# Kernel optimization log

Hardware: AMD Instinct MI355X
Metric: run time of the kernel (lower is better)

Reference implementation:

```python
import jax, jax.numpy as jnp
import numpy as np

D = 64          # dim1 = dim2 = dim3
B = 512         # batch
MMHID = 256
F = (D + 1) ** 3  # 274625, encoder1 input size
SKIP = 3 * (D + 1)  # 195


def _lin(x, w, b):
    # torch nn.Linear: y = x @ W^T + b, W: [out, in]
    return x @ w.T + b


def _bilinear(x1, x2, w, b):
    # torch nn.Bilinear: y_o = x1_i W_{oij} x2_j + b_o
    return jnp.einsum('bi,oij,bj->bo', x1, w, x2) + b


def setup_inputs() -> dict:
    key = jax.random.key(0)
    ks = jax.random.split(key, 16)

    def n(k, shape, scale):
        return (jax.random.normal(k, shape, dtype=jnp.float32) * scale)

    inp = {
        'vec1': n(ks[0], (B, D), 1.0),
        'vec2': n(ks[1], (B, D), 1.0),
        'vec3': n(ks[2], (B, D), 1.0),
        # gated branch 1
        'h1_w': n(ks[3], (D, D), 1.0 / np.sqrt(D)), 'h1_b': jnp.zeros((D,), jnp.float32),
        'z1_w': n(ks[4], (D, D, D), 1.0 / D), 'z1_b': jnp.zeros((D,), jnp.float32),
        'o1_w': n(ks[5], (D, D), 1.0 / np.sqrt(D)), 'o1_b': jnp.zeros((D,), jnp.float32),
        # gated branch 2
        'h2_w': n(ks[6], (D, D), 1.0 / np.sqrt(D)), 'h2_b': jnp.zeros((D,), jnp.float32),
        'z2_w': n(ks[7], (D, D, D), 1.0 / D), 'z2_b': jnp.zeros((D,), jnp.float32),
        'o2_w': n(ks[8], (D, D), 1.0 / np.sqrt(D)), 'o2_b': jnp.zeros((D,), jnp.float32),
        # gated branch 3
        'h3_w': n(ks[9], (D, D), 1.0 / np.sqrt(D)), 'h3_b': jnp.zeros((D,), jnp.float32),
        'z3_w': n(ks[10], (D, D, D), 1.0 / D), 'z3_b': jnp.zeros((D,), jnp.float32),
        'o3_w': n(ks[11], (D, D), 1.0 / np.sqrt(D)), 'o3_b': jnp.zeros((D,), jnp.float32),
        # encoders
        'enc1_w': n(ks[12], (MMHID, F), 1.0 / np.sqrt(F)), 'enc1_b': jnp.zeros((MMHID,), jnp.float32),
        'enc2_w': n(ks[13], (MMHID, MMHID + SKIP), 1.0 / np.sqrt(MMHID + SKIP)), 'enc2_b': jnp.zeros((MMHID,), jnp.float32),
    }
    return inp


def reference(vec1, vec2, vec3,
              h1_w, h1_b, z1_w, z1_b, o1_w, o1_b,
              h2_w, h2_b, z2_w, z2_b, o2_w, o2_b,
              h3_w, h3_b, z3_w, z3_b, o3_w, o3_b,
              enc1_w, enc1_b, enc2_w, enc2_b):
    # dropout layers are identity in eval mode
    h1 = jax.nn.relu(_lin(vec1, h1_w, h1_b))
    z1 = _bilinear(vec1, vec3, z1_w, z1_b)
    o1 = jax.nn.relu(_lin(jax.nn.sigmoid(z1) * h1, o1_w, o1_b))

    h2 = jax.nn.relu(_lin(vec2, h2_w, h2_b))
    z2 = _bilinear(vec2, vec3, z2_w, z2_b)
    o2 = jax.nn.relu(_lin(jax.nn.sigmoid(z2) * h2, o2_w, o2_b))

    h3 = jax.nn.relu(_lin(vec3, h3_w, h3_b))
    z3 = _bilinear(vec1, vec3, z3_w, z3_b)  # note: z3 uses (vec1, vec3) per source
    o3 = jax.nn.relu(_lin(jax.nn.sigmoid(z3) * h3, o3_w, o3_b))

    ones = jnp.ones((o1.shape[0], 1), o1.dtype)
    o1 = jnp.concatenate([o1, ones], axis=1)  # [B, D+1]
    o2 = jnp.concatenate([o2, ones], axis=1)
    o3 = jnp.concatenate([o3, ones], axis=1)

    # trilinear outer product, flattened in (i, j, k) order matching
    # bmm(o1, o2).flatten then bmm(., o3).flatten in torch
    o123 = jnp.einsum('bi,bj,bk->bijk', o1, o2, o3).reshape(o1.shape[0], -1)  # [B, F]

    out = jax.nn.relu(_lin(o123, enc1_w, enc1_b))
    out = jnp.concatenate([out, o1, o2, o3], axis=1)  # skip connection
    out = jax.nn.relu(_lin(out, enc2_w, enc2_b))
    return out
```

## Files before the change

### kernel.cpp

```cpp
#include <hip/hip_runtime.h>
#include <hip/hip_bf16.h>
#include <stdint.h>

typedef unsigned short u16;
typedef unsigned int u32;

#define F1 274625
#define IJ1 4225

typedef float v4f __attribute__((ext_vector_type(4)));
typedef __bf16 v8bf __attribute__((ext_vector_type(8)));

__device__ __forceinline__ float lof(u32 u) { union { u32 u; float f; } c; c.u = u << 16; return c.f; }
__device__ __forceinline__ u16 f2bf(float f) {
  union { float f; u32 u; } c; c.f = f;
  u32 r = (c.u >> 16) & 1u;
  return (u16)((c.u + 0x7fffu + r) >> 16);
}
__device__ __forceinline__ u32 pkbf(u32 a, u32 b) {
  union { float f; u32 u; } ca, cb; ca.u = a; cb.u = b;
  __hip_bfloat162 h = __float22bfloat162_rn(make_float2(ca.f, cb.f));
  union { __hip_bfloat162 h; u32 u; } c; c.h = h; return c.u;
}

__global__ void __launch_bounds__(256) k0_transpose(const float* __restrict__ v1,
    const float* __restrict__ v2, const float* __restrict__ v3, float* __restrict__ xT) {
  int g = blockIdx.x * 256 + threadIdx.x;
  if (g >= 3 * 64 * 512) return;
  int t = g >> 15, r = g & 32767;
  int d = r >> 9, b = r & 511;
  const float* v = (t == 0) ? v1 : ((t == 1) ? v2 : v3);
  xT[g] = v[b * 64 + d];
}

__global__ void __launch_bounds__(256) k1_bilinear(
    const float* __restrict__ zw1, const float* __restrict__ zw2, const float* __restrict__ zw3,
    const float* __restrict__ xT, float* __restrict__ zsum) {
  int bid = blockIdx.x;
  int bh = bid & 1, o = (bid >> 1) & 63, t = bid >> 7;
  int b = bh * 256 + threadIdx.x;
  const float* zw = (t == 0) ? zw1 : ((t == 1) ? zw2 : zw3);
  const float* xiT = xT + ((t == 1) ? 32768 : 0);
  const float* x3T = xT + 65536;
  float x3r[64];
#pragma unroll
  for (int j = 0; j < 64; ++j) x3r[j] = x3T[j * 512 + b];
  const float4* w4 = (const float4*)(zw + o * 4096);
  float acc = 0.f;
#pragma unroll 4
  for (int i = 0; i < 64; ++i) {
    float xi = xiT[i * 512 + b];
    float s = 0.f;
#pragma unroll
    for (int q = 0; q < 16; ++q) {
      float4 w = w4[i * 16 + q];
      s += w.x * x3r[q*4+0] + w.y * x3r[q*4+1] + w.z * x3r[q*4+2] + w.w * x3r[q*4+3];
    }
    acc += xi * s;
  }
  zsum[t * 32768 + o * 512 + b] = acc;
}

__global__ void __launch_bounds__(256) k2_branch(
    const float* __restrict__ hw1, const float* __restrict__ hb1,
    const float* __restrict__ ow1, const float* __restrict__ ob1,
    const float* __restrict__ hw2, const float* __restrict__ hb2,
    const float* __restrict__ ow2, const float* __restrict__ ob2,
    const float* __restrict__ hw3, const float* __restrict__ hb3,
    const float* __restrict__ ow3, const float* __restrict__ ob3,
    const float* __restrict__ zb1, const float* __restrict__ zb2, const float* __restrict__ zb3,
    const float* __restrict__ xT, const float* __restrict__ zsum,
    float* __restrict__ oT, u16* __restrict__ o3row) {
  int t = blockIdx.x >> 3, bc = blockIdx.x & 7;
  int lane = threadIdx.x & 63;
  int w = __builtin_amdgcn_readfirstlane((int)(threadIdx.x >> 6));
  int b = bc * 64 + lane;
  const float* hw = (t==0)?hw1:((t==1)?hw2:hw3);
  const float* hb = (t==0)?hb1:((t==1)?hb2:hb3);
  const float* ow = (t==0)?ow1:((t==1)?ow2:ow3);
  const float* ob = (t==0)?ob1:((t==1)?ob2:ob3);
  const float* zb = (t==0)?zb1:((t==1)?zb2:zb3);
  const float* xtT = xT + t * 32768;
  const float4* hw4 = (const float4*)hw;
  const float4* ow4 = (const float4*)ow;
  __shared__ float gT[64][68];
  float xr[64];
#pragma unroll
  for (int k = 0; k < 64; ++k) xr[k] = xtT[k * 512 + b];
#pragma unroll
  for (int ii = 0; ii < 16; ii += 4) {
    float gv[4];
#pragma unroll
    for (int q = 0; q < 4; ++q) {
      int i = w * 16 + ii + q;
      float a = hb[i];
#pragma unroll
      for (int kq = 0; kq < 16; ++kq) {
        float4 h4 = hw4[i * 16 + kq];
        a += h4.x * xr[kq*4+0] + h4.y * xr[kq*4+1] + h4.z * xr[kq*4+2] + h4.w * xr[kq*4+3];
      }
      float hv = fmaxf(a, 0.f);
      float z = zsum[t * 32768 + i * 512 + b] + zb[i];
      float sg = 1.f / (1.f + __expf(-z));
      gv[q] = sg * hv;
    }
    *(float4*)&gT[lane][w * 16 + ii] = make_float4(gv[0], gv[1], gv[2], gv[3]);
  }
  __syncthreads();
  float gr[64];
#pragma unroll
  for (int k = 0; k < 64; k += 4) {
    float4 g4 = *(const float4*)&gT[lane][k];
    gr[k] = g4.x; gr[k+1] = g4.y; gr[k+2] = g4.z; gr[k+3] = g4.w;
  }
#pragma unroll
  for (int ii = 0; ii < 16; ++ii) {
    int oo = w * 16 + ii;
    float a = ob[oo];
#pragma unroll
    for (int kq = 0; kq < 16; ++kq) {
      float4 o4 = ow4[oo * 16 + kq];
      a += o4.x * gr[kq*4+0] + o4.y * gr[kq*4+1] + o4.z * gr[kq*4+2] + o4.w * gr[kq*4+3];
    }
    float ov = fmaxf(a, 0.f);
    oT[(t * 65 + oo) * 512 + b] = ov;
    if (t == 2) o3row[b * 72 + oo] = f2bf(ov);
  }
  if (w == 0) oT[(t * 65 + 64) * 512 + b] = 1.f;
  if (t == 2 && w == 1) {
    uint4 ones = make_uint4(0x3F80u, 0u, 0u, 0u);
    *(uint4*)&o3row[b * 72 + 64] = ones;
  }
}

template<int S4>
__device__ __forceinline__ void pack_row(const uint4* qv, char* half_base,
                                         char* row_base, int rpos, int hh) {
  u32 l[36];
#pragma unroll
  for (int r = 0; r < 9; ++r) {
    l[4*r+0] = qv[r].x; l[4*r+1] = qv[r].y; l[4*r+2] = qv[r].z; l[4*r+3] = qv[r].w;
  }
#pragma unroll
  for (int cl = 0; cl < 4; ++cl) {
    u32 p0 = pkbf(l[S4+8*cl+0], l[S4+8*cl+1]);
    u32 p1 = pkbf(l[S4+8*cl+2], l[S4+8*cl+3]);
    u32 p2 = pkbf(l[S4+8*cl+4], l[S4+8*cl+5]);
    u32 p3 = pkbf(l[S4+8*cl+6], l[S4+8*cl+7]);
    *(uint4*)(half_base + (((cl + rpos) & 3) * 16)) = make_uint4(p0, p1, p2, p3);
  }
  if (hh) *(u16*)(row_base + 128) = (u16)(pkbf(l[S4+32], l[S4+32]) & 0xffffu);
}

__global__ void __launch_bounds__(256, 2) k4_gemm(
    const float* __restrict__ W, const u16* __restrict__ o3row,
    const float* __restrict__ oT, float* __restrict__ accum,
    float* __restrict__ pbuf, int mode) {
  __shared__ u16 o3r[128 * 72];
  __shared__ u16 Bs[2][128 * 72];
  __shared__ float o12sf[2][128];
  int bid = blockIdx.x;
  int xcd = bid & 7, slot = bid >> 3;
  int mb = slot & 3, ph = slot >> 2;
  int pair = ph * 8 + xcd;
  int sK = pair >> 1, nb = pair & 1;
  int mbase = mb * 128, nbase = nb * 128;
  int ij0 = (sK * IJ1) >> 6, ij1 = ((sK + 1) * IJ1) >> 6;
  int tid = threadIdx.x;
  int lane = tid & 63;
  int wid = __builtin_amdgcn_readfirstlane(tid >> 6);
  int wm = wid >> 1, wn = wid & 1;
  int lrow = lane & 15, lkg = lane >> 4;
  int rpos = lane >> 1, hh = lane & 1;

  v4f acc[16] = {};
  const uint4* Wq = (const uint4*)W;
  uint4 qv[9];
  float cA = 0.f, cB = 0.f;

  auto loadW = [&](int ij) {
    int cc = (wid - ij) & 3;
    int row = rpos * 4 + cc;
    long g = (long)(nbase + row) * F1 + (long)ij * 65;
    long u4 = (g >> 2) + (long)hh * 8;
#pragma unroll
    for (int r = 0; r < 9; ++r) qv[r] = Wq[u4 + r];
  };
  auto loadO = [&](int ij) {
    if (tid < 128) {
      int i = ij / 65, j = ij - i * 65;
      cA = oT[i * 512 + mbase + tid];
      cB = oT[(65 + j) * 512 + mbase + tid];
    }
  };
  auto packCur = [&](int ij, int buf) {
    int cc = (wid - ij) & 3;
    int row = rpos * 4 + cc;
    char* rb = (char*)Bs[buf] + row * 144;
    char* hb = rb + hh * 64;
    if      (wid == 0) pack_row<0>(qv, hb, rb, rpos, hh);
    else if (wid == 1) pack_row<1>(qv, hb, rb, rpos, hh);
    else if (wid == 2) pack_row<2>(qv, hb, rb, rpos, hh);
    else               pack_row<3>(qv, hb, rb, rpos, hh);
    if (tid < 128) o12sf[buf][tid] = cA * cB;
  };

  loadW(ij0); loadO(ij0);

  for (int u = tid; u < 1024; u += 256) {
    int r = u >> 3, c = u & 7;
    uint4 v = *(const uint4*)(o3row + (mbase + r) * 72 + c * 8);
    int half = c >> 2, cl = c & 3;
    int slotc = (cl + (r >> 2)) & 3;
    *(uint4*)((char*)o3r + r * 144 + half * 64 + slotc * 16) = v;
  }

  int rot = ((lkg + (lrow >> 2)) & 3) * 16;
  int aoff[4][2], boff[4][2], vvq[4];
#pragma unroll
  for (int u = 0; u < 4; ++u) {
    int ra = wm * 64 + u * 16 + lrow;
    int rb = wn * 64 + u * 16 + lrow;
#pragma unroll
    for (int k2 = 0; k2 < 2; ++k2) {
      aoff[u][k2] = ra * 144 + k2 * 64 + rot;
      boff[u][k2] = rb * 144 + k2 * 64 + rot;
    }
    vvq[u] = rb * 72 + 64;
  }

  __syncthreads();
  packCur(ij0, 0);
  loadW(ij0 + 1); loadO(ij0 + 1);
  asm volatile("s_waitcnt lgkmcnt(0)\n\ts_barrier" ::: "memory");

#pragma unroll 1
  for (int ij = ij0; ij < ij1; ++ij) {
    int cur = (ij - ij0) & 1;
    if (ij + 1 < ij1) {
      packCur(ij + 1, cur ^ 1);
      if (ij + 2 < ij1) { loadW(ij + 2); loadO(ij + 2); }
    }
    const char* bsC = (const char*)Bs[cur];
    v8bf bfr[4][2];
#pragma unroll
    for (int u2 = 0; u2 < 4; ++u2)
#pragma unroll
      for (int k2 = 0; k2 < 2; ++k2)
        bfr[u2][k2] = *(const v8bf*)(bsC + boff[u2][k2]);
    float vv[4];
#pragma unroll
    for (int u2 = 0; u2 < 4; ++u2) vv[u2] = lof((u32)Bs[cur][vvq[u2]]);
    __builtin_amdgcn_s_setprio(1);
#pragma unroll
    for (int t2 = 0; t2 < 4; ++t2) {
      v8bf a0 = *(const v8bf*)((const char*)o3r + aoff[t2][0]);
      v8bf a1 = *(const v8bf*)((const char*)o3r + aoff[t2][1]);
      v4f P0 = {}, P1 = {}, P2 = {}, P3 = {};
      P0 = __builtin_amdgcn_mfma_f32_16x16x32_bf16(a0, bfr[0][0], P0, 0, 0, 0);
      P0 = __builtin_amdgcn_mfma_f32_16x16x32_bf16(a1, bfr[0][1], P0, 0, 0, 0);
      P1 = __builtin_amdgcn_mfma_f32_16x16x32_bf16(a0, bfr[1][0], P1, 0, 0, 0);
      P1 = __builtin_amdgcn_mfma_f32_16x16x32_bf16(a1, bfr[1][1], P1, 0, 0, 0);
      P2 = __builtin_amdgcn_mfma_f32_16x16x32_bf16(a0, bfr[2][0], P2, 0, 0, 0);
      P2 = __builtin_amdgcn_mfma_f32_16x16x32_bf16(a1, bfr[2][1], P2, 0, 0, 0);
      P3 = __builtin_amdgcn_mfma_f32_16x16x32_bf16(a0, bfr[3][0], P3, 0, 0, 0);
      P3 = __builtin_amdgcn_mfma_f32_16x16x32_bf16(a1, bfr[3][1], P3, 0, 0, 0);
      float4 sp = *(const float4*)&o12sf[cur][wm * 64 + t2 * 16 + lkg * 4];
#pragma unroll
      for (int e = 0; e < 4; ++e) {
        float se = (e == 0) ? sp.x : (e == 1) ? sp.y : (e == 2) ? sp.z : sp.w;
        acc[t2 * 4 + 0][e] += se * (P0[e] + vv[0]);
        acc[t2 * 4 + 1][e] += se * (P1[e] + vv[1]);
        acc[t2 * 4 + 2][e] += se * (P2[e] + vv[2]);
        acc[t2 * 4 + 3][e] += se * (P3[e] + vv[3]);
      }
    }
    __builtin_amdgcn_s_setprio(0);
    asm volatile("s_waitcnt lgkmcnt(0)\n\ts_barrier" ::: "memory");
  }

  if (mode) {
    float* dst = pbuf + ((long)sK << 17);
#pragma unroll
    for (int t2 = 0; t2 < 4; ++t2) {
      int gb0 = mbase + wm * 64 + t2 * 16 + lkg * 4;
#pragma unroll
      for (int u2 = 0; u2 < 4; ++u2) {
        int go = nbase + wn * 64 + u2 * 16 + lrow;
#pragma unroll
        for (int e = 0; e < 4; ++e)
          dst[(gb0 + e) * 256 + go] = acc[t2 * 4 + u2][e];
      }
    }
  } else {
#pragma unroll
    for (int t2 = 0; t2 < 4; ++t2) {
      int gb0 = mbase + wm * 64 + t2 * 16 + lkg * 4;
#pragma unroll
      for (int u2 = 0; u2 < 4; ++u2) {
        int go = nbase + wn * 64 + u2 * 16 + lrow;
#pragma unroll
        for (int e = 0; e < 4; ++e)
          atomicAdd(&accum[(gb0 + e) * 256 + go], acc[t2 * 4 + u2][e]);
      }
    }
  }
}

__global__ void __launch_bounds__(256) k4_reduce(const float* __restrict__ P,
    const float* __restrict__ e1b, float* __restrict__ xrT) {
  int g = blockIdx.x * 256 + threadIdx.x;
  const v4f* p4 = (const v4f*)P;
  v4f s = p4[g];
#pragma unroll 4
  for (int k = 1; k < 64; ++k) s += p4[(k << 15) + g];
  int b = g >> 6, c0 = (g & 63) << 2;
#pragma unroll
  for (int e = 0; e < 4; ++e)
    xrT[(c0 + e) * 512 + b] = fmaxf(s[e] + e1b[c0 + e], 0.f);
}

__global__ void __launch_bounds__(256) k5_enc2(
    const float* __restrict__ xin, const float* __restrict__ oT,
    const float* __restrict__ enc1b, const float* __restrict__ w2,
    const float* __restrict__ enc2b, float* __restrict__ outp, int mode) {
  int bg = blockIdx.x >> 3, og = blockIdx.x & 7;
  int lane = threadIdx.x & 63;
  int w = __builtin_amdgcn_readfirstlane((int)(threadIdx.x >> 6));
  int b = bg * 64 + lane;
  int obase = og * 32 + w * 8;
  float a8[8];
#pragma unroll
  for (int q = 0; q < 8; ++q) a8[q] = enc2b[obase + q];
  if (mode) {
    for (int c = 0; c < 256; ++c) {
      float x = xin[c * 512 + b];
#pragma unroll
      for (int q = 0; q < 8; ++q) a8[q] += w2[(obase + q) * 451 + c] * x;
    }
  } else {
    for (int c = 0; c < 256; ++c) {
      float x = fmaxf(xin[b * 256 + c] + enc1b[c], 0.f);
#pragma unroll
      for (int q = 0; q < 8; ++q) a8[q] += w2[(obase + q) * 451 + c] * x;
    }
  }
  for (int e = 0; e < 195; ++e) {
    float x = oT[e * 512 + b];
#pragma unroll
    for (int q = 0; q < 8; ++q) a8[q] += w2[(obase + q) * 451 + 256 + e] * x;
  }
#pragma unroll
  for (int q = 0; q < 8; ++q) outp[b * 256 + obase + q] = fmaxf(a8[q], 0.f);
}

extern "C" void kernel_launch(void* const* d_in, const int* in_sizes, int n_in,
                              void* d_out, int out_size, void* d_ws, size_t ws_size,
                              hipStream_t stream) {
  const float* vec1 = (const float*)d_in[0];
  const float* vec2 = (const float*)d_in[1];
  const float* vec3 = (const float*)d_in[2];
  const float* h1w = (const float*)d_in[3];  const float* h1b = (const float*)d_in[4];
  const float* z1w = (const float*)d_in[5];  const float* z1b = (const float*)d_in[6];
  const float* o1w = (const float*)d_in[7];  const float* o1b = (const float*)d_in[8];
  const float* h2w = (const float*)d_in[9];  const float* h2b = (const float*)d_in[10];
  const float* z2w = (const float*)d_in[11]; const float* z2b = (const float*)d_in[12];
  const float* o2w = (const float*)d_in[13]; const float* o2b = (const float*)d_in[14];
  const float* h3w = (const float*)d_in[15]; const float* h3b = (const float*)d_in[16];
  const float* z3w = (const float*)d_in[17]; const float* z3b = (const float*)d_in[18];
  const float* o3w = (const float*)d_in[19]; const float* o3b = (const float*)d_in[20];
  const float* e1w = (const float*)d_in[21]; const float* e1b = (const float*)d_in[22];
  const float* e2w = (const float*)d_in[23]; const float* e2b = (const float*)d_in[24];

  char* ws = (char*)d_ws;
  float* accum = (float*)(ws + 0);
  float* oT    = (float*)(ws + 524288);
  u16* o3row   = (u16*)  (ws + 923648);
  float* xT    = (float*)(ws + 997376);
  float* zsum  = (float*)(ws + 1390592);
  float* pbuf  = (float*)(ws + 1783808);
  size_t need = 1783808 + (size_t)64 * 512 * 256 * 4;
  int mode = (ws_size >= need) ? 1 : 0;
  float* pArg = mode ? pbuf : accum;

  if (!mode) hipMemsetAsync(accum, 0, 524288, stream);

  hipLaunchKernelGGL(k0_transpose, dim3(384), dim3(256), 0, stream, vec1, vec2, vec3, xT);
  hipLaunchKernelGGL(k1_bilinear, dim3(384), dim3(256), 0, stream,
                     z1w, z2w, z3w, xT, zsum);
  hipLaunchKernelGGL(k2_branch, dim3(24), dim3(256), 0, stream,
                     h1w, h1b, o1w, o1b, h2w, h2b, o2w, o2b, h3w, h3b, o3w, o3b,
                     z1b, z2b, z3b, xT, zsum, oT, o3row);
  hipLaunchKernelGGL(k4_gemm, dim3(512), dim3(256), 0, stream, e1w, o3row, oT, accum,
                     pArg, mode);
  if (mode)
    hipLaunchKernelGGL(k4_reduce, dim3(128), dim3(256), 0, stream, pbuf, e1b, accum);
  hipLaunchKernelGGL(k5_enc2, dim3(64), dim3(256), 0, stream, accum, oT, e1b, e2w, e2b,
                     (float*)d_out, mode);
}
```

Before: 750.2 us.

## Deepen GEMM weight prefetch, swizzle LDS layout, split bilinear, transpose enc2 weights

The main enc1 GEMM now double-buffers weight registers so loads run two steps ahead of packing, and uses an unpadded XOR-style swizzled LDS layout with the extra column stored separately. The bilinear kernel is split in half over the input dimension to double the grid, with partial sums added in the branch kernel. A new kernel transposes enc2 weights so a new enc2 kernel can read them coalesced, with batch inputs staged in shared memory. This adds register pressure and extra launches in exchange for more latency hiding and better memory access patterns.

```diff
diff --git a/kernel.cpp b/kernel.cpp
--- a/kernel.cpp
+++ b/kernel.cpp
@@ -33,11 +33,31 @@
   xT[g] = v[b * 64 + d];
 }
 
+__global__ void __launch_bounds__(256) k3t_w2t(const float* __restrict__ w2,
+                                               float* __restrict__ w2T) {
+  __shared__ float t[32][33];
+  int bx = blockIdx.x & 7, by = blockIdx.x >> 3;
+  int tx = threadIdx.x & 31, ty = threadIdx.x >> 5;
+  int c = by * 32 + tx;
+#pragma unroll
+  for (int r = 0; r < 32; r += 8) {
+    int o = bx * 32 + ty + r;
+    t[ty + r][tx] = (c < 451) ? w2[o * 451 + c] : 0.f;
+  }
+  __syncthreads();
+#pragma unroll
+  for (int r = 0; r < 32; r += 8) {
+    int cc = by * 32 + ty + r;
+    if (cc < 451) w2T[cc * 256 + bx * 32 + tx] = t[tx][ty + r];
+  }
+}
+
 __global__ void __launch_bounds__(256) k1_bilinear(
     const float* __restrict__ zw1, const float* __restrict__ zw2, const float* __restrict__ zw3,
     const float* __restrict__ xT, float* __restrict__ zsum) {
   int bid = blockIdx.x;
-  int bh = bid & 1, o = (bid >> 1) & 63, t = bid >> 7;
+  int ih = bid & 1, bh = (bid >> 1) & 1;
+  int o = (bid >> 2) & 63, t = bid >> 8;
   int b = bh * 256 + threadIdx.x;
   const float* zw = (t == 0) ? zw1 : ((t == 1) ? zw2 : zw3);
   const float* xiT = xT + ((t == 1) ? 32768 : 0);
@@ -47,8 +67,9 @@
   for (int j = 0; j < 64; ++j) x3r[j] = x3T[j * 512 + b];
   const float4* w4 = (const float4*)(zw + o * 4096);
   float acc = 0.f;
+  int i0 = ih * 32;
 #pragma unroll 4
-  for (int i = 0; i < 64; ++i) {
+  for (int i = i0; i < i0 + 32; ++i) {
     float xi = xiT[i * 512 + b];
     float s = 0.f;
 #pragma unroll
@@ -58,7 +79,7 @@
     }
     acc += xi * s;
   }
-  zsum[t * 32768 + o * 512 + b] = acc;
+  zsum[ih * 98304 + t * 32768 + o * 512 + b] = acc;
 }
 
 __global__ void __launch_bounds__(256) k2_branch(
@@ -100,7 +121,8 @@
         a += h4.x * xr[kq*4+0] + h4.y * xr[kq*4+1] + h4.z * xr[kq*4+2] + h4.w * xr[kq*4+3];
       }
       float hv = fmaxf(a, 0.f);
-      float z = zsum[t * 32768 + i * 512 + b] + zb[i];
+      int zi = t * 32768 + i * 512 + b;
+      float z = zsum[zi] + zsum[98304 + zi] + zb[i];
       float sg = 1.f / (1.f + __expf(-z));
       gv[q] = sg * hv;
     }
@@ -134,30 +156,33 @@
 }
 
 template<int S4>
-__device__ __forceinline__ void pack_row(const uint4* qv, char* half_base,
-                                         char* row_base, int rpos, int hh) {
+__device__ __forceinline__ void pack_row(const uint4* qv, u16* bp, u16* vvp,
+                                         int row, int hh) {
   u32 l[36];
 #pragma unroll
   for (int r = 0; r < 9; ++r) {
     l[4*r+0] = qv[r].x; l[4*r+1] = qv[r].y; l[4*r+2] = qv[r].z; l[4*r+3] = qv[r].w;
   }
+  int rp = (row >> 2) + 2 * (row & 3);
 #pragma unroll
   for (int cl = 0; cl < 4; ++cl) {
     u32 p0 = pkbf(l[S4+8*cl+0], l[S4+8*cl+1]);
     u32 p1 = pkbf(l[S4+8*cl+2], l[S4+8*cl+3]);
     u32 p2 = pkbf(l[S4+8*cl+4], l[S4+8*cl+5]);
     u32 p3 = pkbf(l[S4+8*cl+6], l[S4+8*cl+7]);
-    *(uint4*)(half_base + (((cl + rpos) & 3) * 16)) = make_uint4(p0, p1, p2, p3);
-  }
-  if (hh) *(u16*)(row_base + 128) = (u16)(pkbf(l[S4+32], l[S4+32]) & 0xffffu);
+    int pos = (hh * 4 + cl + rp) & 7;
+    *(uint4*)(bp + (pos << 3)) = make_uint4(p0, p1, p2, p3);
+  }
+  if (hh) vvp[row] = (u16)(pkbf(l[S4+32], l[S4+32]) & 0xffffu);
 }
 
 __global__ void __launch_bounds__(256, 2) k4_gemm(
     const float* __restrict__ W, const u16* __restrict__ o3row,
     const float* __restrict__ oT, float* __restrict__ accum,
     float* __restrict__ pbuf, int mode) {
-  __shared__ u16 o3r[128 * 72];
-  __shared__ u16 Bs[2][128 * 72];
+  __shared__ u16 o3r[128 * 64];
+  __shared__ u16 Bs[2][128 * 64];
+  __shared__ u16 vvs[2][128];
   __shared__ float o12sf[2][128];
   int bid = blockIdx.x;
   int xcd = bid & 7, slot = bid >> 3;
@@ -175,87 +200,91 @@
 
   v4f acc[16] = {};
   const uint4* Wq = (const uint4*)W;
-  uint4 qv[9];
-  float cA = 0.f, cB = 0.f;
-
-  auto loadW = [&](int ij) {
+  uint4 qa[9], qb[9];
+  float aA = 0.f, aB = 0.f, bA = 0.f, bB = 0.f;
+
+  auto loadW = [&](int ij, uint4* q) {
     int cc = (wid - ij) & 3;
     int row = rpos * 4 + cc;
     long g = (long)(nbase + row) * F1 + (long)ij * 65;
     long u4 = (g >> 2) + (long)hh * 8;
 #pragma unroll
-    for (int r = 0; r < 9; ++r) qv[r] = Wq[u4 + r];
+    for (int r = 0; r < 9; ++r) q[r] = Wq[u4 + r];
   };
-  auto loadO = [&](int ij) {
+  auto loadO = [&](int ij, float& A, float& B) {
     if (tid < 128) {
       int i = ij / 65, j = ij - i * 65;
-      cA = oT[i * 512 + mbase + tid];
-      cB = oT[(65 + j) * 512 + mbase + tid];
+      A = oT[i * 512 + mbase + tid];
+      B = oT[(65 + j) * 512 + mbase + tid];
     }
   };
-  auto packCur = [&](int ij, int buf) {
+  auto packCur = [&](int ij, int buf, const uint4* q, float pA, float pB) {
     int cc = (wid - ij) & 3;
     int row = rpos * 4 + cc;
-    char* rb = (char*)Bs[buf] + row * 144;
-    char* hb = rb + hh * 64;
-    if      (wid == 0) pack_row<0>(qv, hb, rb, rpos, hh);
-    else if (wid == 1) pack_row<1>(qv, hb, rb, rpos, hh);
-    else if (wid == 2) pack_row<2>(qv, hb, rb, rpos, hh);
-    else               pack_row<3>(qv, hb, rb, rpos, hh);
-    if (tid < 128) o12sf[buf][tid] = cA * cB;
+    u16* bp = &Bs[buf][row << 6];
+    if      (wid == 0) pack_row<0>(q, bp, &vvs[buf][0], row, hh);
+    else if (wid == 1) pack_row<1>(q, bp, &vvs[buf][0], row, hh);
+    else if (wid == 2) pack_row<2>(q, bp, &vvs[buf][0], row, hh);
+    else               pack_row<3>(q, bp, &vvs[buf][0], row, hh);
+    if (tid < 128) o12sf[buf][tid] = pA * pB;
   };
 
-  loadW(ij0); loadO(ij0);
+  loadW(ij0, qa); loadO(ij0, aA, aB);
 
   for (int u = tid; u < 1024; u += 256) {
     int r = u >> 3, c = u & 7;
     uint4 v = *(const uint4*)(o3row + (mbase + r) * 72 + c * 8);
-    int half = c >> 2, cl = c & 3;
-    int slotc = (cl + (r >> 2)) & 3;
-    *(uint4*)((char*)o3r + r * 144 + half * 64 + slotc * 16) = v;
-  }
-
-  int rot = ((lkg + (lrow >> 2)) & 3) * 16;
-  int aoff[4][2], boff[4][2], vvq[4];
+    int pos = (c + (r >> 2) + 2 * (r & 3)) & 7;
+    *(uint4*)&o3r[(r << 6) + (pos << 3)] = v;
+  }
+
+  loadW(ij0 + 1, qb); loadO(ij0 + 1, bA, bB);
+
+  int aoff[4][2], boff[4][2], vvr[4];
 #pragma unroll
   for (int u = 0; u < 4; ++u) {
     int ra = wm * 64 + u * 16 + lrow;
     int rb = wn * 64 + u * 16 + lrow;
 #pragma unroll
     for (int k2 = 0; k2 < 2; ++k2) {
-      aoff[u][k2] = ra * 144 + k2 * 64 + rot;
-      boff[u][k2] = rb * 144 + k2 * 64 + rot;
-    }
-    vvq[u] = rb * 72 + 64;
+      aoff[u][k2] = (ra << 6) + (((k2 * 4 + lkg + (ra >> 2) + 2 * (ra & 3)) & 7) << 3);
+      boff[u][k2] = (rb << 6) + (((k2 * 4 + lkg + (rb >> 2) + 2 * (rb & 3)) & 7) << 3);
+    }
+    vvr[u] = rb;
   }
 
   __syncthreads();
-  packCur(ij0, 0);
-  loadW(ij0 + 1); loadO(ij0 + 1);
+  packCur(ij0, 0, qa, aA, aB);
+  loadW(ij0 + 2, qa); loadO(ij0 + 2, aA, aB);
   asm volatile("s_waitcnt lgkmcnt(0)\n\ts_barrier" ::: "memory");
 
 #pragma unroll 1
   for (int ij = ij0; ij < ij1; ++ij) {
     int cur = (ij - ij0) & 1;
     if (ij + 1 < ij1) {
-      packCur(ij + 1, cur ^ 1);
-      if (ij + 2 < ij1) { loadW(ij + 2); loadO(ij + 2); }
-    }
-    const char* bsC = (const char*)Bs[cur];
+      if (cur == 0) {
+        packCur(ij + 1, 1, qb, bA, bB);
+        if (ij + 3 < ij1) { loadW(ij + 3, qb); loadO(ij + 3, bA, bB); }
+      } else {
+        packCur(ij + 1, 0, qa, aA, aB);
+        if (ij + 3 < ij1) { loadW(ij + 3, qa); loadO(ij + 3, aA, aB); }
+      }
+    }
+    const u16* bs = Bs[cur];
     v8bf bfr[4][2];
 #pragma unroll
     for (int u2 = 0; u2 < 4; ++u2)
 #pragma unroll
       for (int k2 = 0; k2 < 2; ++k2)
-        bfr[u2][k2] = *(const v8bf*)(bsC + boff[u2][k2]);
+        bfr[u2][k2] = *(const v8bf*)&bs[boff[u2][k2]];
     float vv[4];
 #pragma unroll
-    for (int u2 = 0; u2 < 4; ++u2) vv[u2] = lof((u32)Bs[cur][vvq[u2]]);
+    for (int u2 = 0; u2 < 4; ++u2) vv[u2] = lof((u32)vvs[cur][vvr[u2]]);
     __builtin_amdgcn_s_setprio(1);
 #pragma unroll
     for (int t2 = 0; t2 < 4; ++t2) {
-      v8bf a0 = *(const v8bf*)((const char*)o3r + aoff[t2][0]);
-      v8bf a1 = *(const v8bf*)((const char*)o3r + aoff[t2][1]);
+      v8bf a0 = *(const v8bf*)&o3r[aoff[t2][0]];
+      v8bf a1 = *(const v8bf*)&o3r[aoff[t2][1]];
       v4f P0 = {}, P1 = {}, P2 = {}, P3 = {};
       P0 = __builtin_amdgcn_mfma_f32_16x16x32_bf16(a0, bfr[0][0], P0, 0, 0, 0);
       P0 = __builtin_amdgcn_mfma_f32_16x16x32_bf16(a1, bfr[0][1], P0, 0, 0, 0);
@@ -320,10 +349,37 @@
     xrT[(c0 + e) * 512 + b] = fmaxf(s[e] + e1b[c0 + e], 0.f);
 }
 
+__global__ void __launch_bounds__(256) k5v_enc2(const float* __restrict__ xrT,
+    const float* __restrict__ oT, const float* __restrict__ w2T,
+    const float* __restrict__ enc2b, float* __restrict__ outp) {
+  __shared__ float xl[451 * 8 + 8];
+  int b0 = blockIdx.x * 8;
+  int tid = threadIdx.x;
+  for (int u = tid; u < 3608; u += 256) {
+    int c = u >> 3, bi = u & 7;
+    xl[u] = (c < 256) ? xrT[c * 512 + b0 + bi] : oT[(c - 256) * 512 + b0 + bi];
+  }
+  float a[8];
+  float bv = enc2b[tid];
+#pragma unroll
+  for (int q = 0; q < 8; ++q) a[q] = bv;
+  __syncthreads();
+#pragma unroll 4
+  for (int c = 0; c < 451; ++c) {
+    float w = w2T[c * 256 + tid];
+    float4 x0 = *(const float4*)&xl[c * 8];
+    float4 x1 = *(const float4*)&xl[c * 8 + 4];
+    a[0] += w * x0.x; a[1] += w * x0.y; a[2] += w * x0.z; a[3] += w * x0.w;
+    a[4] += w * x1.x; a[5] += w * x1.y; a[6] += w * x1.z; a[7] += w * x1.w;
+  }
+#pragma unroll
+  for (int q = 0; q < 8; ++q) outp[(b0 + q) * 256 + tid] = fmaxf(a[q], 0.f);
+}
+
 __global__ void __launch_bounds__(256) k5_enc2(
     const float* __restrict__ xin, const float* __restrict__ oT,
     const float* __restrict__ enc1b, const float* __restrict__ w2,
-    const float* __restrict__ enc2b, float* __restrict__ outp, int mode) {
+    const float* __restrict__ enc2b, float* __restrict__ outp) {
   int bg = blockIdx.x >> 3, og = blockIdx.x & 7;
   int lane = threadIdx.x & 63;
   int w = __builtin_amdgcn_readfirstlane((int)(threadIdx.x >> 6));
@@ -332,18 +388,10 @@
   float a8[8];
 #pragma unroll
   for (int q = 0; q < 8; ++q) a8[q] = enc2b[obase + q];
-  if (mode) {
-    for (int c = 0; c < 256; ++c) {
-      float x = xin[c * 512 + b];
-#pragma unroll
-      for (int q = 0; q < 8; ++q) a8[q] += w2[(obase + q) * 451 + c] * x;
-    }
-  } else {
-    for (int c = 0; c < 256; ++c) {
-      float x = fmaxf(xin[b * 256 + c] + enc1b[c], 0.f);
-#pragma unroll
-      for (int q = 0; q < 8; ++q) a8[q] += w2[(obase + q) * 451 + c] * x;
-    }
+  for (int c = 0; c < 256; ++c) {
+    float x = fmaxf(xin[b * 256 + c] + enc1b[c], 0.f);
+#pragma unroll
+    for (int q = 0; q < 8; ++q) a8[q] += w2[(obase + q) * 451 + c] * x;
   }
   for (int e = 0; e < 195; ++e) {
     float x = oT[e * 512 + b];
@@ -378,23 +426,30 @@
   u16* o3row   = (u16*)  (ws + 923648);
   float* xT    = (float*)(ws + 997376);
   float* zsum  = (float*)(ws + 1390592);
-  float* pbuf  = (float*)(ws + 1783808);
-  size_t need = 1783808 + (size_t)64 * 512 * 256 * 4;
+  float* w2T   = (float*)(ws + 2177024);
+  float* pbuf  = (float*)(ws + 2638848);
+  size_t need = 2638848 + (size_t)64 * 512 * 256 * 4;
   int mode = (ws_size >= need) ? 1 : 0;
   float* pArg = mode ? pbuf : accum;
 
   if (!mode) hipMemsetAsync(accum, 0, 524288, stream);
 
   hipLaunchKernelGGL(k0_transpose, dim3(384), dim3(256), 0, stream, vec1, vec2, vec3, xT);
-  hipLaunchKernelGGL(k1_bilinear, dim3(384), dim3(256), 0, stream,
+  if (mode)
+    hipLaunchKernelGGL(k3t_w2t, dim3(120), dim3(256), 0, stream, e2w, w2T);
+  hipLaunchKernelGGL(k1_bilinear, dim3(768), dim3(256), 0, stream,
                      z1w, z2w, z3w, xT, zsum);
   hipLaunchKernelGGL(k2_branch, dim3(24), dim3(256), 0, stream,
                      h1w, h1b, o1w, o1b, h2w, h2b, o2w, o2b, h3w, h3b, o3w, o3b,
                      z1b, z2b, z3b, xT, zsum, oT, o3row);
   hipLaunchKernelGGL(k4_gemm, dim3(512), dim3(256), 0, stream, e1w, o3row, oT, accum,
                      pArg, mode);
-  if (mode)
+  if (mode) {
     hipLaunchKernelGGL(k4_reduce, dim3(128), dim3(256), 0, stream, pbuf, e1b, accum);
-  hipLaunchKernelGGL(k5_enc2, dim3(64), dim3(256), 0, stream, accum, oT, e1b, e2w, e2b,
-                     (float*)d_out, mode);
-}
+    hipLaunchKernelGGL(k5v_enc2, dim3(64), dim3(256), 0, stream, accum, oT, w2T, e2b,
+                       (float*)d_out);
+  } else {
+    hipLaunchKernelGGL(k5_enc2, dim3(64), dim3(256), 0, stream, accum, oT, e1b, e2w, e2b,
+                       (float*)d_out);
+  }
+}
```

Result: no change. 738.4 us (-1.6%).
